# Optimization experiments

Hardware: AMD Instinct MI355X
Metric: run time of the kernel (lower is better)

## Reference

```python
import jax, jax.numpy as jnp
import numpy as np

N_GENES = 15135
K = int(np.ceil(0.5 * N_GENES))  # 7568, PyG TopKPooling ratio=0.5
BS, E, F_IN, H, HF, NC, L = 8, 242160, 64, 128, 512, 2, 3


def setup_inputs() -> dict:
    key = jax.random.key(0)
    ks = jax.random.split(key, 16)
    def lin(k, fin, fout):
        s = 1.0 / np.sqrt(fin)
        return jax.random.normal(k, (fin, fout), jnp.float32) * s
    x = jax.random.normal(ks[0], (BS, N_GENES, F_IN), jnp.float32)
    batch = jnp.zeros((BS,), jnp.int32)
    edge_index = jax.random.randint(ks[1], (2, E), 0, N_GENES, dtype=jnp.int32)
    CAT = L * H
    return {
        "x": x,
        "batch": batch,
        "edge_index": edge_index,
        "W1": lin(ks[2], F_IN, H), "b1": jnp.zeros((H,), jnp.float32),
        "W2": lin(ks[3], H, H),    "b2": jnp.zeros((H,), jnp.float32),
        "W3": lin(ks[4], H, H),    "b3": jnp.zeros((H,), jnp.float32),
        "topk_w": jax.random.normal(ks[5], (CAT,), jnp.float32) / np.sqrt(CAT),
        "fcW": lin(ks[6], CAT, 1), "fcb": jnp.zeros((1,), jnp.float32),
        "lin1W": lin(ks[7], K, HF), "lin1b": jnp.zeros((HF,), jnp.float32),
        "lin2W": lin(ks[8], HF, NC), "lin2b": jnp.zeros((NC,), jnp.float32),
    }


def reference(x, batch, edge_index, W1, b1, W2, b2, W3, b3,
              topk_w, fcW, fcb, lin1W, lin1b, lin2W, lin2b):
    bs = x.shape[0]
    # --- GCN normalization with self-loops (PyG GCNConv defaults) ---
    loop = jnp.arange(N_GENES, dtype=edge_index.dtype)
    src = jnp.concatenate([edge_index[0], loop])
    dst = jnp.concatenate([edge_index[1], loop])
    deg = jnp.zeros((N_GENES,), x.dtype).at[dst].add(1.0)
    dinv = jax.lax.rsqrt(deg)  # deg >= 1 due to self-loops
    norm = dinv[src] * dinv[dst]  # [E+N]

    def gcn(h, W, b):
        h = h @ W                                   # [bs, N, H]
        msg = h[:, src, :] * norm[None, :, None]    # gather + edge weight
        agg = jnp.zeros_like(h).at[:, dst, :].add(msg)  # scatter-add
        return agg + b

    h1 = jax.nn.relu(gcn(x, W1, b1))
    h2 = jax.nn.relu(gcn(h1, W2, b2))
    h3 = jax.nn.relu(gcn(h2, W3, b3))
    # mode='cat': stack on last dim then flatten -> feature order (H, layer)
    xc = jnp.stack([h1, h2, h3], -1).reshape(bs, N_GENES, -1)  # [bs, N, L*H]

    # --- TopKPooling (score = tanh(x.w/||w||), keep top ceil(0.5*N)) ---
    score = jnp.tanh((xc @ topk_w) / jnp.linalg.norm(topk_w))  # [bs, N]
    top_s, perm = jax.lax.top_k(score, K)                       # [bs, K]
    xp = jnp.take_along_axis(xc, perm[..., None], axis=1) * top_s[..., None]

    z = (xp @ fcW + fcb)[..., 0]          # [bs, K]
    h = jax.nn.relu(z @ lin1W + lin1b)    # [bs, HF]; dropout inactive (eval)
    logits = h @ lin2W + lin2b            # [bs, NC]
    return jax.nn.log_softmax(logits, axis=-1)
```

## Files before the change

kernel.cpp:

```cpp
#include <hip/hip_runtime.h>

#define N_G   15135
#define E_N   242160
#define BSZ   8
#define K_TOP 7568
#define NH    128
#define NBIN  65536
#define SUFS  65600

typedef float f4v __attribute__((ext_vector_type(4)));

__global__ void zero_kernel(int* __restrict__ p, int n) {
  int i = blockIdx.x * 1024 + threadIdx.x;
  if (i < n) p[i] = 0;
}

__global__ void count_kernel(const int* __restrict__ ei, int* __restrict__ cnt) {
  int e = blockIdx.x * 256 + threadIdx.x;
  if (e < E_N) atomicAdd(&cnt[ei[E_N + e]], 1);
}

__global__ __launch_bounds__(1024) void scan_kernel(const int* __restrict__ cnt,
                                                    int* __restrict__ rowstart,
                                                    float* __restrict__ dinv,
                                                    int4* __restrict__ rowdesc,
                                                    int* __restrict__ gctr,
                                                    const float* __restrict__ topk_w,
                                                    float* __restrict__ scal) {
  __shared__ int buf[1024];
  __shared__ int base;
  int tid = threadIdx.x;
  int i = blockIdx.x * 1024 + tid;
  int v = (i < N_G) ? cnt[i] : 0;
  float di = 1.0f / sqrtf((float)(v + 1));
  if (i < N_G) dinv[i] = di;
  buf[tid] = v;
  __syncthreads();
  for (int s = 1; s < 1024; s <<= 1) {
    int t = (tid >= s) ? buf[tid - s] : 0;
    __syncthreads();
    buf[tid] += t;
    __syncthreads();
  }
  if (tid == 1023) base = atomicAdd(gctr, buf[1023]);
  __syncthreads();
  if (i < N_G) {
    int rs = base + buf[tid] - v;
    rowstart[i] = rs;
    rowdesc[i] = make_int4(rs, v, __float_as_int(di), 0);
  }
  if (blockIdx.x == 0) {
    __shared__ float fbuf[512];
    if (tid < 512) {
      float w = (tid < 384) ? topk_w[tid] : 0.f;
      fbuf[tid] = w * w;
    }
    __syncthreads();
    for (int s = 256; s > 0; s >>= 1) {
      if (tid < s) fbuf[tid] += fbuf[tid + s];
      __syncthreads();
    }
    if (tid == 0) scal[0] = 1.0f / sqrtf(fbuf[0]);
  }
}

__global__ void fill_kernel(const int* __restrict__ ei, const int* __restrict__ rowstart,
                            const float* __restrict__ dinv, int* __restrict__ fillc,
                            int2* __restrict__ csr) {
  int e = blockIdx.x * 256 + threadIdx.x;
  if (e < E_N) {
    int s = ei[e], d = ei[E_N + e];
    int pos = rowstart[d] + atomicAdd(&fillc[d], 1);
    csr[pos] = make_int2(s, __float_as_int(dinv[s]));
  }
}

template<int CIN, bool BR>
__global__ __launch_bounds__(256, 6) void mm_kernel(const float* __restrict__ A,
                                                    const float* __restrict__ W,
                                                    const float* __restrict__ bias,
                                                    float* __restrict__ out) {
  __shared__ float Bst[32][132];
  __shared__ float Ast2[32][68];
  int tid = threadIdx.x;
  int b = blockIdx.x & 7;
  int ib = blockIdx.x >> 3;
  int rb0 = b * N_G + ib * 64;
  int rmax = N_G - ib * 64;
  int c0 = (tid & 31) * 4;
  int r0 = (tid >> 5) * 8;
  float acc[8][4];
#pragma unroll
  for (int i = 0; i < 8; i++)
#pragma unroll
    for (int j = 0; j < 4; j++) acc[i][j] = 0.f;

  for (int k0 = 0; k0 < CIN; k0 += 32) {
    {
      int koff = (tid & 7) * 4;
      int row = tid >> 3;
#pragma unroll
      for (int p = 0; p < 2; ++p) {
        int r = row + p * 32;
        f4v v = {0.f, 0.f, 0.f, 0.f};
        if (r < rmax) v = __builtin_nontemporal_load((const f4v*)(A + (size_t)(rb0 + r) * CIN + k0 + koff));
        Ast2[koff + 0][r] = v.x; Ast2[koff + 1][r] = v.y;
        Ast2[koff + 2][r] = v.z; Ast2[koff + 3][r] = v.w;
      }
    }
    {
      int cc = (tid & 31) * 4;
      int kr = tid >> 5;
#pragma unroll
      for (int p = 0; p < 4; ++p) {
        int k = kr + p * 8;
        *(float4*)&Bst[k][cc] = *(const float4*)(W + (size_t)(k0 + k) * NH + cc);
      }
    }
    __syncthreads();
#pragma unroll 4
    for (int kk = 0; kk < 32; ++kk) {
      float a[8], bb[4];
      *(float4*)&a[0] = *(const float4*)&Ast2[kk][r0];
      *(float4*)&a[4] = *(const float4*)&Ast2[kk][r0 + 4];
      *(float4*)&bb[0] = *(const float4*)&Bst[kk][c0];
#pragma unroll
      for (int i = 0; i < 8; i++)
#pragma unroll
        for (int j = 0; j < 4; j++)
          acc[i][j] = fmaf(a[i], bb[j], acc[i][j]);
    }
    __syncthreads();
  }
  float b0 = 0.f, b1 = 0.f, b2 = 0.f, b3 = 0.f;
  if (BR) { b0 = bias[c0]; b1 = bias[c0+1]; b2 = bias[c0+2]; b3 = bias[c0+3]; }
#pragma unroll
  for (int i = 0; i < 8; i++) {
    int r = r0 + i;
    if (r < rmax) {
      float4 v;
      if (BR) {
        v.x = fmaxf(acc[i][0] + b0, 0.f); v.y = fmaxf(acc[i][1] + b1, 0.f);
        v.z = fmaxf(acc[i][2] + b2, 0.f); v.w = fmaxf(acc[i][3] + b3, 0.f);
      } else {
        v.x = acc[i][0]; v.y = acc[i][1]; v.z = acc[i][2]; v.w = acc[i][3];
      }
      *(float4*)(out + (size_t)(rb0 + r) * NH + c0) = v;
    }
  }
}

__global__ __launch_bounds__(256) void agg64_f4_kernel(const float* __restrict__ src,
                                                       const int2* __restrict__ csr,
                                                       const int4* __restrict__ rowdesc,
                                                       float* __restrict__ dst) {
  int b = blockIdx.x & 7;
  int chunk = blockIdx.x >> 3;
  int wave = threadIdx.x >> 6, lane = threadIdx.x & 63;
  int d = chunk * 4 + wave;
  if (d >= N_G) return;
  d = __builtin_amdgcn_readfirstlane(d);
  int slot = lane >> 4, li = lane & 15;
  int4 rd = rowdesc[d];
  int n = rd.y;
  float dv = __int_as_float(rd.z);
  const float* sb = src + (size_t)b * N_G * 64;
  const int2* ce = csr + rd.x;
  auto sel4 = [&](int a0, int a1, int a2, int a3) {
    int s01 = (slot & 1) ? a1 : a0;
    int s23 = (slot & 1) ? a3 : a2;
    return (slot & 2) ? s23 : s01;
  };
  f4v acc0 = {0.f, 0.f, 0.f, 0.f}, acc1 = {0.f, 0.f, 0.f, 0.f};
  {
    f4v sv = *(const f4v*)(sb + (size_t)d * 64 + li * 4);
    float ws = (slot == 0) ? dv : 0.f;
    acc0.x = fmaf(ws, sv.x, acc0.x); acc0.y = fmaf(ws, sv.y, acc0.y);
    acc0.z = fmaf(ws, sv.z, acc0.z); acc0.w = fmaf(ws, sv.w, acc0.w);
  }
  int l = 0;
  for (; l + 8 <= n; l += 8) {
    int2 p[8];
#pragma unroll
    for (int k = 0; k < 8; ++k) p[k] = ce[l + k];
    int s0 = sel4(p[0].x, p[1].x, p[2].x, p[3].x);
    int s1 = sel4(p[4].x, p[5].x, p[6].x, p[7].x);
    float w0 = __int_as_float(sel4(p[0].y, p[1].y, p[2].y, p[3].y));
    float w1 = __int_as_float(sel4(p[4].y, p[5].y, p[6].y, p[7].y));
    f4v v0 = *(const f4v*)(sb + (size_t)s0 * 64 + li * 4);
    f4v v1 = *(const f4v*)(sb + (size_t)s1 * 64 + li * 4);
    acc0.x = fmaf(w0, v0.x, acc0.x); acc0.y = fmaf(w0, v0.y, acc0.y);
    acc0.z = fmaf(w0, v0.z, acc0.z); acc0.w = fmaf(w0, v0.w, acc0.w);
    acc1.x = fmaf(w1, v1.x, acc1.x); acc1.y = fmaf(w1, v1.y, acc1.y);
    acc1.z = fmaf(w1, v1.z, acc1.z); acc1.w = fmaf(w1, v1.w, acc1.w);
  }
  for (; l < n; ++l) {
    int2 p = ce[l];
    float w = (slot == 0) ? __int_as_float(p.y) : 0.f;
    f4v v = *(const f4v*)(sb + (size_t)p.x * 64 + li * 4);
    acc0.x = fmaf(w, v.x, acc0.x); acc0.y = fmaf(w, v.y, acc0.y);
    acc0.z = fmaf(w, v.z, acc0.z); acc0.w = fmaf(w, v.w, acc0.w);
  }
  f4v a;
  a.x = acc0.x + acc1.x; a.y = acc0.y + acc1.y;
  a.z = acc0.z + acc1.z; a.w = acc0.w + acc1.w;
  a.x += __shfl_xor(a.x, 16); a.y += __shfl_xor(a.y, 16);
  a.z += __shfl_xor(a.z, 16); a.w += __shfl_xor(a.w, 16);
  a.x += __shfl_xor(a.x, 32); a.y += __shfl_xor(a.y, 32);
  a.z += __shfl_xor(a.z, 32); a.w += __shfl_xor(a.w, 32);
  if (slot == 0) {
    f4v r;
    r.x = dv * a.x; r.y = dv * a.y; r.z = dv * a.z; r.w = dv * a.w;
    __builtin_nontemporal_store(r, (f4v*)(dst + ((size_t)b * N_G + d) * 64 + li * 4));
  }
}

template<int MODE>
__global__ __launch_bounds__(256) void agg128_f4_kernel(const float* __restrict__ hw,
                                                        const int2* __restrict__ csr,
                                                        const int4* __restrict__ rowdesc,
                                                        const float* __restrict__ bias,
                                                        const float* __restrict__ h1,
                                                        const float* __restrict__ h2,
                                                        const float* __restrict__ topk_w,
                                                        const float* __restrict__ fcW,
                                                        const float* __restrict__ scal,
                                                        float* __restrict__ hout,
                                                        float* __restrict__ score,
                                                        float* __restrict__ d2a,
                                                        unsigned* __restrict__ keys,
                                                        int* __restrict__ hist) {
  int b = blockIdx.x & 7;
  int chunk = blockIdx.x >> 3;
  int wave = threadIdx.x >> 6, lane = threadIdx.x & 63;
  int d0 = chunk * 8 + wave * 2;
  if (d0 >= N_G) return;
  d0 = __builtin_amdgcn_readfirstlane(d0);
  int d1i = d0 + 1;
  int has1 = (d1i < N_G);
  int dB = has1 ? d1i : d0;
  int half = lane >> 5, li = lane & 31;
  int4 rdA = rowdesc[d0];
  int4 rdB = rowdesc[dB];
  int nA = rdA.y, nB = has1 ? rdB.y : 0;
  float dvA = __int_as_float(rdA.z);
  float dvB = __int_as_float(rdB.z);
  const float* sb = hw + (size_t)b * N_G * NH;
  const int2* ceA = csr + rdA.x;
  const int2* ceB = csr + rdB.x;
  auto sel2 = [&](int a0, int a1) { return half ? a1 : a0; };
  f4v aA0 = {0.f,0.f,0.f,0.f}, aA1 = {0.f,0.f,0.f,0.f};
  f4v aB0 = {0.f,0.f,0.f,0.f}, aB1 = {0.f,0.f,0.f,0.f};
  {
    f4v sv = *(const f4v*)(sb + (size_t)d0 * NH + li * 4);
    float ws = (half == 0) ? dvA : 0.f;
    aA0.x = fmaf(ws, sv.x, aA0.x); aA0.y = fmaf(ws, sv.y, aA0.y);
    aA0.z = fmaf(ws, sv.z, aA0.z); aA0.w = fmaf(ws, sv.w, aA0.w);
    f4v svb = *(const f4v*)(sb + (size_t)dB * NH + li * 4);
    float wsb = (half == 0 && has1) ? dvB : 0.f;
    aB0.x = fmaf(wsb, svb.x, aB0.x); aB0.y = fmaf(wsb, svb.y, aB0.y);
    aB0.z = fmaf(wsb, svb.z, aB0.z); aB0.w = fmaf(wsb, svb.w, aB0.w);
  }
  auto batch8 = [&](const int2* ce, int l, f4v& c0, f4v& c1) {
    int2 p[8];
#pragma unroll
    for (int k = 0; k < 8; ++k) p[k] = ce[l + k];
    int s0 = sel2(p[0].x, p[1].x), s1 = sel2(p[2].x, p[3].x);
    int s2 = sel2(p[4].x, p[5].x), s3 = sel2(p[6].x, p[7].x);
    float w0 = __int_as_float(sel2(p[0].y, p[1].y));
    float w1 = __int_as_float(sel2(p[2].y, p[3].y));
    float w2 = __int_as_float(sel2(p[4].y, p[5].y));
    float w3 = __int_as_float(sel2(p[6].y, p[7].y));
    f4v v0 = *(const f4v*)(sb + (size_t)s0 * NH + li * 4);
    f4v v1 = *(const f4v*)(sb + (size_t)s1 * NH + li * 4);
    f4v v2 = *(const f4v*)(sb + (size_t)s2 * NH + li * 4);
    f4v v3 = *(const f4v*)(sb + (size_t)s3 * NH + li * 4);
    c0.x = fmaf(w0, v0.x, c0.x); c0.y = fmaf(w0, v0.y, c0.y);
    c0.z = fmaf(w0, v0.z, c0.z); c0.w = fmaf(w0, v0.w, c0.w);
    c1.x = fmaf(w1, v1.x, c1.x); c1.y = fmaf(w1, v1.y, c1.y);
    c1.z = fmaf(w1, v1.z, c1.z); c1.w = fmaf(w1, v1.w, c1.w);
    c0.x = fmaf(w2, v2.x, c0.x); c0.y = fmaf(w2, v2.y, c0.y);
    c0.z = fmaf(w2, v2.z, c0.z); c0.w = fmaf(w2, v2.w, c0.w);
    c1.x = fmaf(w3, v3.x, c1.x); c1.y = fmaf(w3, v3.y, c1.y);
    c1.z = fmaf(w3, v3.z, c1.z); c1.w = fmaf(w3, v3.w, c1.w);
  };
  int lA = 0, lB = 0;
  while (lA + 8 <= nA && lB + 8 <= nB) {
    int2 pA[8], pB[8];
#pragma unroll
    for (int k = 0; k < 8; ++k) pA[k] = ceA[lA + k];
#pragma unroll
    for (int k = 0; k < 8; ++k) pB[k] = ceB[lB + k];
    int sa0 = sel2(pA[0].x, pA[1].x), sa1 = sel2(pA[2].x, pA[3].x);
    int sa2 = sel2(pA[4].x, pA[5].x), sa3 = sel2(pA[6].x, pA[7].x);
    int sb0_ = sel2(pB[0].x, pB[1].x), sb1_ = sel2(pB[2].x, pB[3].x);
    int sb2_ = sel2(pB[4].x, pB[5].x), sb3_ = sel2(pB[6].x, pB[7].x);
    float wa0 = __int_as_float(sel2(pA[0].y, pA[1].y));
    float wa1 = __int_as_float(sel2(pA[2].y, pA[3].y));
    float wa2 = __int_as_float(sel2(pA[4].y, pA[5].y));
    float wa3 = __int_as_float(sel2(pA[6].y, pA[7].y));
    float wb0 = __int_as_float(sel2(pB[0].y, pB[1].y));
    float wb1 = __int_as_float(sel2(pB[2].y, pB[3].y));
    float wb2 = __int_as_float(sel2(pB[4].y, pB[5].y));
    float wb3 = __int_as_float(sel2(pB[6].y, pB[7].y));
    f4v va0 = *(const f4v*)(sb + (size_t)sa0 * NH + li * 4);
    f4v va1 = *(const f4v*)(sb + (size_t)sa1 * NH + li * 4);
    f4v va2 = *(const f4v*)(sb + (size_t)sa2 * NH + li * 4);
    f4v va3 = *(const f4v*)(sb + (size_t)sa3 * NH + li * 4);
    f4v vb0 = *(const f4v*)(sb + (size_t)sb0_ * NH + li * 4);
    f4v vb1 = *(const f4v*)(sb + (size_t)sb1_ * NH + li * 4);
    f4v vb2 = *(const f4v*)(sb + (size_t)sb2_ * NH + li * 4);
    f4v vb3 = *(const f4v*)(sb + (size_t)sb3_ * NH + li * 4);
    aA0.x = fmaf(wa0, va0.x, aA0.x); aA0.y = fmaf(wa0, va0.y, aA0.y);
    aA0.z = fmaf(wa0, va0.z, aA0.z); aA0.w = fmaf(wa0, va0.w, aA0.w);
    aA1.x = fmaf(wa1, va1.x, aA1.x); aA1.y = fmaf(wa1, va1.y, aA1.y);
    aA1.z = fmaf(wa1, va1.z, aA1.z); aA1.w = fmaf(wa1, va1.w, aA1.w);
    aA0.x = fmaf(wa2, va2.x, aA0.x); aA0.y = fmaf(wa2, va2.y, aA0.y);
    aA0.z = fmaf(wa2, va2.z, aA0.z); aA0.w = fmaf(wa2, va2.w, aA0.w);
    aA1.x = fmaf(wa3, va3.x, aA1.x); aA1.y = fmaf(wa3, va3.y, aA1.y);
    aA1.z = fmaf(wa3, va3.z, aA1.z); aA1.w = fmaf(wa3, va3.w, aA1.w);
    aB0.x = fmaf(wb0, vb0.x, aB0.x); aB0.y = fmaf(wb0, vb0.y, aB0.y);
    aB0.z = fmaf(wb0, vb0.z, aB0.z); aB0.w = fmaf(wb0, vb0.w, aB0.w);
    aB1.x = fmaf(wb1, vb1.x, aB1.x); aB1.y = fmaf(wb1, vb1.y, aB1.y);
    aB1.z = fmaf(wb1, vb1.z, aB1.z); aB1.w = fmaf(wb1, vb1.w, aB1.w);
    aB0.x = fmaf(wb2, vb2.x, aB0.x); aB0.y = fmaf(wb2, vb2.y, aB0.y);
    aB0.z = fmaf(wb2, vb2.z, aB0.z); aB0.w = fmaf(wb2, vb2.w, aB0.w);
    aB1.x = fmaf(wb3, vb3.x, aB1.x); aB1.y = fmaf(wb3, vb3.y, aB1.y);
    aB1.z = fmaf(wb3, vb3.z, aB1.z); aB1.w = fmaf(wb3, vb3.w, aB1.w);
    lA += 8; lB += 8;
  }
  for (; lA + 8 <= nA; lA += 8) batch8(ceA, lA, aA0, aA1);
  for (; lB + 8 <= nB; lB += 8) batch8(ceB, lB, aB0, aB1);
  while (lA < nA || lB < nB) {
    int hasA = (lA < nA), hasB = (lB < nB);
    int sA = hasA ? ceA[lA].x : d0;
    int wAi = hasA ? ceA[lA].y : 0;
    int sB = hasB ? ceB[lB].x : d0;
    int wBi = hasB ? ceB[lB].y : 0;
    int s = half ? sB : sA;
    float wa = (half == 0 && hasA) ? __int_as_float(wAi) : 0.f;
    float wb = (half == 1 && hasB) ? __int_as_float(wBi) : 0.f;
    f4v v = *(const f4v*)(sb + (size_t)s * NH + li * 4);
    aA0.x = fmaf(wa, v.x, aA0.x); aA0.y = fmaf(wa, v.y, aA0.y);
    aA0.z = fmaf(wa, v.z, aA0.z); aA0.w = fmaf(wa, v.w, aA0.w);
    aB0.x = fmaf(wb, v.x, aB0.x); aB0.y = fmaf(wb, v.y, aB0.y);
    aB0.z = fmaf(wb, v.z, aB0.z); aB0.w = fmaf(wb, v.w, aB0.w);
    lA += hasA; lB += hasB;
  }
  f4v aA, aB;
  aA.x = aA0.x + aA1.x; aA.y = aA0.y + aA1.y;
  aA.z = aA0.z + aA1.z; aA.w = aA0.w + aA1.w;
  aB.x = aB0.x + aB1.x; aB.y = aB0.y + aB1.y;
  aB.z = aB0.z + aB1.z; aB.w = aB0.w + aB1.w;
  aA.x += __shfl_xor(aA.x, 32); aA.y += __shfl_xor(aA.y, 32);
  aA.z += __shfl_xor(aA.z, 32); aA.w += __shfl_xor(aA.w, 32);
  aB.x += __shfl_xor(aB.x, 32); aB.y += __shfl_xor(aB.y, 32);
  aB.z += __shfl_xor(aB.z, 32); aB.w += __shfl_xor(aB.w, 32);

  f4v bb = *(const f4v*)(bias + li * 4);
  float dv = half ? dvB : dvA;
  f4v av;
  av.x = half ? aB.x : aA.x; av.y = half ? aB.y : aA.y;
  av.z = half ? aB.z : aA.z; av.w = half ? aB.w : aA.w;
  f4v r;
  r.x = fmaxf(fmaf(dv, av.x, bb.x), 0.f);
  r.y = fmaxf(fmaf(dv, av.y, bb.y), 0.f);
  r.z = fmaxf(fmaf(dv, av.z, bb.z), 0.f);
  r.w = fmaxf(fmaf(dv, av.w, bb.w), 0.f);
  int dsel = half ? dB : d0;

  if constexpr (MODE == 0) {
    if (half == 0 || has1)
      __builtin_nontemporal_store(r, (f4v*)(hout + ((size_t)b * N_G + dsel) * NH + li * 4));
  } else {
    size_t rb = ((size_t)b * N_G + dsel) * NH + li * 4;
    f4v u1 = __builtin_nontemporal_load((const f4v*)(h1 + rb));
    f4v u2 = __builtin_nontemporal_load((const f4v*)(h2 + rb));
    const float* twp = topk_w + li * 12;
    const float* fwp = fcW + li * 12;
    f4v ta = *(const f4v*)(twp + 0), tb2 = *(const f4v*)(twp + 4), tc = *(const f4v*)(twp + 8);
    f4v fa = *(const f4v*)(fwp + 0), fb = *(const f4v*)(fwp + 4), fc = *(const f4v*)(fwp + 8);
    float d1 = u1.x * ta.x + u2.x * ta.y + r.x * ta.z
             + u1.y * ta.w + u2.y * tb2.x + r.y * tb2.y
             + u1.z * tb2.z + u2.z * tb2.w + r.z * tc.x
             + u1.w * tc.y + u2.w * tc.z + r.w * tc.w;
    float d2 = u1.x * fa.x + u2.x * fa.y + r.x * fa.z
             + u1.y * fa.w + u2.y * fb.x + r.y * fb.y
             + u1.z * fb.z + u2.z * fb.w + r.z * fc.x
             + u1.w * fc.y + u2.w * fc.z + r.w * fc.w;
#pragma unroll
    for (int sh = 16; sh > 0; sh >>= 1) {
      d1 += __shfl_down(d1, sh, 32);
      d2 += __shfl_down(d2, sh, 32);
    }
    if (li == 0 && (half == 0 || has1)) {
      int gw = b * N_G + dsel;
      float scv = tanhf(d1 * scal[0]);
      score[gw] = scv;
      d2a[gw] = d2;
      unsigned u = __float_as_uint(scv);
      unsigned k32 = (u & 0x80000000u) ? ~u : (u | 0x80000000u);
      keys[gw] = k32;
      atomicAdd(&hist[b * NBIN + (int)(k32 >> 16)], 1);
    }
  }
}

__global__ __launch_bounds__(1024) void suffix_kernel(const int* __restrict__ hist,
                                                      int* __restrict__ suf) {
  __shared__ int buf[1024];
  int b = blockIdx.x;
  const int* hb = hist + b * NBIN;
  int* sb = suf + b * SUFS;
  int t = threadIdx.x;
  int base = t * 64;
  int s = 0;
  for (int k = 0; k < 64; ++k) s += hb[base + k];
  buf[t] = s;
  __syncthreads();
  for (int off = 1; off < 1024; off <<= 1) {
    int v = (t + off < 1024) ? buf[t + off] : 0;
    __syncthreads();
    buf[t] += v;
    __syncthreads();
  }
  int acc = buf[t] - s;
  if (t == 0) sb[NBIN] = 0;
  for (int k = 63; k >= 0; --k) {
    acc += hb[base + k];
    sb[base + k] = acc;
  }
}

__global__ void scatter_kernel(const unsigned* __restrict__ keys, int* __restrict__ hist,
                               const int* __restrict__ suf, int2* __restrict__ bucket) {
  int b = blockIdx.y;
  int i = blockIdx.x * 256 + threadIdx.x;
  if (i >= N_G) return;
  unsigned k = keys[b * N_G + i];
  int bin = (int)(k >> 16);
  int old = atomicSub(&hist[b * NBIN + bin], 1);
  int pos = suf[b * SUFS + bin + 1] + old - 1;
  bucket[b * N_G + pos] = make_int2((int)k, i);
}

__global__ void rank_z_kernel(const unsigned* __restrict__ keys, const int* __restrict__ suf,
                              const int2* __restrict__ bucket, const float* __restrict__ score,
                              const float* __restrict__ d2a, const float* __restrict__ fcb,
                              float* __restrict__ z) {
  int b = blockIdx.y;
  int i = blockIdx.x * 256 + threadIdx.x;
  if (i >= N_G) return;
  int gw = b * N_G + i;
  unsigned k = keys[gw];
  int bin = (int)(k >> 16);
  int lo = suf[b * SUFS + bin + 1];
  int hi = suf[b * SUFS + bin];
  int r = lo;
  const int2* bk = bucket + b * N_G;
  for (int p = lo; p < hi; ++p) {
    int2 e = bk[p];
    unsigned kj = (unsigned)e.x;
    r += (kj > k || (kj == k && e.y < i)) ? 1 : 0;
  }
  if (r < K_TOP) z[b * K_TOP + r] = fmaf(score[gw], d2a[gw], fcb[0]);
}

__global__ __launch_bounds__(256) void lin1_kernel(const float* __restrict__ z,
                                                   const float* __restrict__ W,
                                                   float* __restrict__ hpre) {
  __shared__ float zb[237];
  int b = blockIdx.y, rs = blockIdx.x;
  int r0 = rs * 237;
  int rn = K_TOP - r0; if (rn > 237) rn = 237;
  for (int q = threadIdx.x; q < rn; q += 256) zb[q] = z[b * K_TOP + r0 + q];
  __syncthreads();
  int c = threadIdx.x;
  float a0 = 0.f, a1 = 0.f;
  for (int r = 0; r < rn; ++r) {
    float zz = zb[r];
    const float* wr = W + (size_t)(r0 + r) * 512;
    a0 = fmaf(zz, wr[c], a0);
    a1 = fmaf(zz, wr[c + 256], a1);
  }
  atomicAdd(&hpre[b * 512 + c], a0);
  atomicAdd(&hpre[b * 512 + c + 256], a1);
}

__global__ __launch_bounds__(128) void lin2_kernel(const float* __restrict__ hpre,
                                                   const float* __restrict__ l1b,
                                                   const float* __restrict__ W2,
                                                   const float* __restrict__ l2b,
                                                   float* __restrict__ out) {
  int b = blockIdx.x, tid = threadIdx.x;
  float a0 = 0.f, a1 = 0.f;
  for (int j = tid; j < 512; j += 128) {
    float t = fmaxf(hpre[b * 512 + j] + l1b[j], 0.f);
    a0 = fmaf(t, W2[j * 2 + 0], a0);
    a1 = fmaf(t, W2[j * 2 + 1], a1);
  }
#pragma unroll
  for (int s = 32; s > 0; s >>= 1) {
    a0 += __shfl_down(a0, s);
    a1 += __shfl_down(a1, s);
  }
  __shared__ float red[2][2];
  if ((tid & 63) == 0) { red[tid >> 6][0] = a0; red[tid >> 6][1] = a1; }
  __syncthreads();
  if (tid == 0) {
    float l0 = red[0][0] + red[1][0] + l2b[0];
    float l1 = red[0][1] + red[1][1] + l2b[1];
    float m = fmaxf(l0, l1);
    float lse = m + logf(expf(l0 - m) + expf(l1 - m));
    out[b * 2 + 0] = l0 - lse;
    out[b * 2 + 1] = l1 - lse;
  }
}

extern "C" void kernel_launch(void* const* d_in, const int* in_sizes, int n_in,
                              void* d_out, int out_size, void* d_ws, size_t ws_size,
                              hipStream_t stream) {
  const float* x   = (const float*)d_in[0];
  const int*   ei  = (const int*)d_in[2];
  const float* W1  = (const float*)d_in[3];
  const float* b1  = (const float*)d_in[4];
  const float* W2  = (const float*)d_in[5];
  const float* b2  = (const float*)d_in[6];
  const float* W3  = (const float*)d_in[7];
  const float* b3  = (const float*)d_in[8];
  const float* tkw = (const float*)d_in[9];
  const float* fcW = (const float*)d_in[10];
  const float* fcb = (const float*)d_in[11];
  const float* l1W = (const float*)d_in[12];
  const float* l1b = (const float*)d_in[13];
  const float* l2W = (const float*)d_in[14];
  const float* l2b = (const float*)d_in[15];
  float* out = (float*)d_out;

  char* ws = (char*)d_ws;
  size_t off = 0;
  auto alloc = [&](size_t bytes) {
    char* p = ws + off;
    off += (bytes + 255) & ~(size_t)255;
    return p;
  };
  int*   cnt   = (int*)alloc(15136 * 4);
  int*   fillc = (int*)alloc(15136 * 4);
  int*   gctr  = (int*)alloc(256);
  float* hpre  = (float*)alloc(4096 * 4);
  int*   hist  = (int*)alloc((size_t)BSZ * NBIN * 4);
  int*   rowstart = (int*)alloc(15136 * 4);
  float* dinv  = (float*)alloc(15136 * 4);
  int4*  rowdesc = (int4*)alloc(15136 * 16);
  float* scal  = (float*)alloc(64);
  float* z     = (float*)alloc((size_t)BSZ * K_TOP * 4);
  float* score = (float*)alloc(121088 * 4);
  float* d2a   = (float*)alloc(121088 * 4);
  unsigned* keys = (unsigned*)alloc(121088 * 4);
  int*   suf   = (int*)alloc((size_t)BSZ * SUFS * 4);
  int2*  bucket = (int2*)alloc(121088 * 8);
  int2*  csr   = (int2*)alloc((size_t)E_N * 8);
  float* ax = (float*)alloc((size_t)BSZ * N_G * 64 * 4);
  float* hw = (float*)alloc((size_t)BSZ * N_G * NH * 4);
  float* h1 = (float*)alloc((size_t)BSZ * N_G * NH * 4);
  float* h2 = (float*)alloc((size_t)BSZ * N_G * NH * 4);
  (void)ws_size; (void)in_sizes; (void)n_in; (void)out_size;

  int zero_n = (int)(((char*)rowstart - (char*)cnt) / 4);
  zero_kernel<<<(zero_n + 1023) / 1024, 1024, 0, stream>>>(cnt, zero_n);
  count_kernel<<<(E_N + 255) / 256, 256, 0, stream>>>(ei, cnt);
  scan_kernel<<<(N_G + 1023) / 1024, 1024, 0, stream>>>(cnt, rowstart, dinv, rowdesc, gctr, tkw, scal);
  fill_kernel<<<(E_N + 255) / 256, 256, 0, stream>>>(ei, rowstart, dinv, fillc, csr);

  dim3 mmg(8 * 237);
  int aggblocks  = 8 * ((N_G + 3) / 4);
  int aggblocks2 = 8 * ((N_G + 7) / 8);

  agg64_f4_kernel<<<aggblocks, 256, 0, stream>>>(x, csr, rowdesc, ax);
  mm_kernel<64, true><<<mmg, 256, 0, stream>>>(ax, W1, b1, h1);
  mm_kernel<128, false><<<mmg, 256, 0, stream>>>(h1, W2, nullptr, hw);
  agg128_f4_kernel<0><<<aggblocks2, 256, 0, stream>>>(hw, csr, rowdesc, b2,
                                                      nullptr, nullptr, nullptr, nullptr, nullptr,
                                                      h2, nullptr, nullptr, nullptr, nullptr);
  mm_kernel<128, false><<<mmg, 256, 0, stream>>>(h2, W3, nullptr, hw);
  agg128_f4_kernel<1><<<aggblocks2, 256, 0, stream>>>(hw, csr, rowdesc, b3,
                                                      h1, h2, tkw, fcW, scal,
                                                      nullptr, score, d2a, keys, hist);

  dim3 ng((N_G + 255) / 256, BSZ);
  suffix_kernel<<<BSZ, 1024, 0, stream>>>(hist, suf);
  scatter_kernel<<<ng, 256, 0, stream>>>(keys, hist, suf, bucket);
  rank_z_kernel<<<ng, 256, 0, stream>>>(keys, suf, bucket, score, d2a, fcb, z);

  dim3 l1g(32, BSZ);
  lin1_kernel<<<l1g, 256, 0, stream>>>(z, l1W, hpre);
  lin2_kernel<<<BSZ, 128, 0, stream>>>(hpre, l1b, l2W, l2b, out);
}
```

Measured before the change: 616.8 us.

## Store layer-3 transform in fp16 and batch lin1 across graphs

The third GCN layer's matmul output is written as fp16, and a new aggregation+score kernel gathers fp16 rows, so gather traffic for that layer is halved. It processes one node per wave with 16-lane slots and four edges in flight. lin1 now handles all 8 batch rows per block, so each weight row is read once instead of eight times. The agg128 kernel is simplified to its non-score mode. The fp16 intermediate reduces precision and could perturb top-k ordering near ties.

```diff
diff --git a/kernel.cpp b/kernel.cpp
--- a/kernel.cpp
+++ b/kernel.cpp
@@ -1,4 +1,5 @@
 #include <hip/hip_runtime.h>
+#include <hip/hip_fp16.h>
 
 #define N_G   15135
 #define E_N   242160
@@ -9,6 +10,7 @@
 #define SUFS  65600
 
 typedef float f4v __attribute__((ext_vector_type(4)));
+typedef unsigned int u4v __attribute__((ext_vector_type(4)));
 
 __global__ void zero_kernel(int* __restrict__ p, int n) {
   int i = blockIdx.x * 1024 + threadIdx.x;
@@ -75,11 +77,11 @@
   }
 }
 
-template<int CIN, bool BR>
+template<int CIN, bool BR, bool H16>
 __global__ __launch_bounds__(256, 6) void mm_kernel(const float* __restrict__ A,
                                                     const float* __restrict__ W,
                                                     const float* __restrict__ bias,
-                                                    float* __restrict__ out) {
+                                                    void* __restrict__ outv) {
   __shared__ float Bst[32][132];
   __shared__ float Ast2[32][68];
   int tid = threadIdx.x;
@@ -138,14 +140,21 @@
   for (int i = 0; i < 8; i++) {
     int r = r0 + i;
     if (r < rmax) {
-      float4 v;
-      if (BR) {
-        v.x = fmaxf(acc[i][0] + b0, 0.f); v.y = fmaxf(acc[i][1] + b1, 0.f);
-        v.z = fmaxf(acc[i][2] + b2, 0.f); v.w = fmaxf(acc[i][3] + b3, 0.f);
+      if (H16) {
+        __half2 pr[2];
+        pr[0] = __floats2half2_rn(acc[i][0], acc[i][1]);
+        pr[1] = __floats2half2_rn(acc[i][2], acc[i][3]);
+        *(uint2*)((__half*)outv + (size_t)(rb0 + r) * NH + c0) = *(uint2*)pr;
       } else {
-        v.x = acc[i][0]; v.y = acc[i][1]; v.z = acc[i][2]; v.w = acc[i][3];
+        float4 v;
+        if (BR) {
+          v.x = fmaxf(acc[i][0] + b0, 0.f); v.y = fmaxf(acc[i][1] + b1, 0.f);
+          v.z = fmaxf(acc[i][2] + b2, 0.f); v.w = fmaxf(acc[i][3] + b3, 0.f);
+        } else {
+          v.x = acc[i][0]; v.y = acc[i][1]; v.z = acc[i][2]; v.w = acc[i][3];
+        }
+        *(float4*)((float*)outv + (size_t)(rb0 + r) * NH + c0) = v;
       }
-      *(float4*)(out + (size_t)(rb0 + r) * NH + c0) = v;
     }
   }
 }
@@ -215,21 +224,11 @@
   }
 }
 
-template<int MODE>
 __global__ __launch_bounds__(256) void agg128_f4_kernel(const float* __restrict__ hw,
                                                         const int2* __restrict__ csr,
                                                         const int4* __restrict__ rowdesc,
                                                         const float* __restrict__ bias,
-                                                        const float* __restrict__ h1,
-                                                        const float* __restrict__ h2,
-                                                        const float* __restrict__ topk_w,
-                                                        const float* __restrict__ fcW,
-                                                        const float* __restrict__ scal,
-                                                        float* __restrict__ hout,
-                                                        float* __restrict__ score,
-                                                        float* __restrict__ d2a,
-                                                        unsigned* __restrict__ keys,
-                                                        int* __restrict__ hist) {
+                                                        float* __restrict__ hout) {
   int b = blockIdx.x & 7;
   int chunk = blockIdx.x >> 3;
   int wave = threadIdx.x >> 6, lane = threadIdx.x & 63;
@@ -286,47 +285,8 @@
   };
   int lA = 0, lB = 0;
   while (lA + 8 <= nA && lB + 8 <= nB) {
-    int2 pA[8], pB[8];
-#pragma unroll
-    for (int k = 0; k < 8; ++k) pA[k] = ceA[lA + k];
-#pragma unroll
-    for (int k = 0; k < 8; ++k) pB[k] = ceB[lB + k];
-    int sa0 = sel2(pA[0].x, pA[1].x), sa1 = sel2(pA[2].x, pA[3].x);
-    int sa2 = sel2(pA[4].x, pA[5].x), sa3 = sel2(pA[6].x, pA[7].x);
-    int sb0_ = sel2(pB[0].x, pB[1].x), sb1_ = sel2(pB[2].x, pB[3].x);
-    int sb2_ = sel2(pB[4].x, pB[5].x), sb3_ = sel2(pB[6].x, pB[7].x);
-    float wa0 = __int_as_float(sel2(pA[0].y, pA[1].y));
-    float wa1 = __int_as_float(sel2(pA[2].y, pA[3].y));
-    float wa2 = __int_as_float(sel2(pA[4].y, pA[5].y));
-    float wa3 = __int_as_float(sel2(pA[6].y, pA[7].y));
-    float wb0 = __int_as_float(sel2(pB[0].y, pB[1].y));
-    float wb1 = __int_as_float(sel2(pB[2].y, pB[3].y));
-    float wb2 = __int_as_float(sel2(pB[4].y, pB[5].y));
-    float wb3 = __int_as_float(sel2(pB[6].y, pB[7].y));
-    f4v va0 = *(const f4v*)(sb + (size_t)sa0 * NH + li * 4);
-    f4v va1 = *(const f4v*)(sb + (size_t)sa1 * NH + li * 4);
-    f4v va2 = *(const f4v*)(sb + (size_t)sa2 * NH + li * 4);
-    f4v va3 = *(const f4v*)(sb + (size_t)sa3 * NH + li * 4);
-    f4v vb0 = *(const f4v*)(sb + (size_t)sb0_ * NH + li * 4);
-    f4v vb1 = *(const f4v*)(sb + (size_t)sb1_ * NH + li * 4);
-    f4v vb2 = *(const f4v*)(sb + (size_t)sb2_ * NH + li * 4);
-    f4v vb3 = *(const f4v*)(sb + (size_t)sb3_ * NH + li * 4);
-    aA0.x = fmaf(wa0, va0.x, aA0.x); aA0.y = fmaf(wa0, va0.y, aA0.y);
-    aA0.z = fmaf(wa0, va0.z, aA0.z); aA0.w = fmaf(wa0, va0.w, aA0.w);
-    aA1.x = fmaf(wa1, va1.x, aA1.x); aA1.y = fmaf(wa1, va1.y, aA1.y);
-    aA1.z = fmaf(wa1, va1.z, aA1.z); aA1.w = fmaf(wa1, va1.w, aA1.w);
-    aA0.x = fmaf(wa2, va2.x, aA0.x); aA0.y = fmaf(wa2, va2.y, aA0.y);
-    aA0.z = fmaf(wa2, va2.z, aA0.z); aA0.w = fmaf(wa2, va2.w, aA0.w);
-    aA1.x = fmaf(wa3, va3.x, aA1.x); aA1.y = fmaf(wa3, va3.y, aA1.y);
-    aA1.z = fmaf(wa3, va3.z, aA1.z); aA1.w = fmaf(wa3, va3.w, aA1.w);
-    aB0.x = fmaf(wb0, vb0.x, aB0.x); aB0.y = fmaf(wb0, vb0.y, aB0.y);
-    aB0.z = fmaf(wb0, vb0.z, aB0.z); aB0.w = fmaf(wb0, vb0.w, aB0.w);
-    aB1.x = fmaf(wb1, vb1.x, aB1.x); aB1.y = fmaf(wb1, vb1.y, aB1.y);
-    aB1.z = fmaf(wb1, vb1.z, aB1.z); aB1.w = fmaf(wb1, vb1.w, aB1.w);
-    aB0.x = fmaf(wb2, vb2.x, aB0.x); aB0.y = fmaf(wb2, vb2.y, aB0.y);
-    aB0.z = fmaf(wb2, vb2.z, aB0.z); aB0.w = fmaf(wb2, vb2.w, aB0.w);
-    aB1.x = fmaf(wb3, vb3.x, aB1.x); aB1.y = fmaf(wb3, vb3.y, aB1.y);
-    aB1.z = fmaf(wb3, vb3.z, aB1.z); aB1.w = fmaf(wb3, vb3.w, aB1.w);
+    batch8(ceA, lA, aA0, aA1);
+    batch8(ceB, lB, aB0, aB1);
     lA += 8; lB += 8;
   }
   for (; lA + 8 <= nA; lA += 8) batch8(ceA, lA, aA0, aA1);
@@ -368,41 +328,120 @@
   r.z = fmaxf(fmaf(dv, av.z, bb.z), 0.f);
   r.w = fmaxf(fmaf(dv, av.w, bb.w), 0.f);
   int dsel = half ? dB : d0;
-
-  if constexpr (MODE == 0) {
-    if (half == 0 || has1)
-      __builtin_nontemporal_store(r, (f4v*)(hout + ((size_t)b * N_G + dsel) * NH + li * 4));
-  } else {
-    size_t rb = ((size_t)b * N_G + dsel) * NH + li * 4;
-    f4v u1 = __builtin_nontemporal_load((const f4v*)(h1 + rb));
-    f4v u2 = __builtin_nontemporal_load((const f4v*)(h2 + rb));
-    const float* twp = topk_w + li * 12;
-    const float* fwp = fcW + li * 12;
-    f4v ta = *(const f4v*)(twp + 0), tb2 = *(const f4v*)(twp + 4), tc = *(const f4v*)(twp + 8);
-    f4v fa = *(const f4v*)(fwp + 0), fb = *(const f4v*)(fwp + 4), fc = *(const f4v*)(fwp + 8);
-    float d1 = u1.x * ta.x + u2.x * ta.y + r.x * ta.z
-             + u1.y * ta.w + u2.y * tb2.x + r.y * tb2.y
-             + u1.z * tb2.z + u2.z * tb2.w + r.z * tc.x
-             + u1.w * tc.y + u2.w * tc.z + r.w * tc.w;
-    float d2 = u1.x * fa.x + u2.x * fa.y + r.x * fa.z
-             + u1.y * fa.w + u2.y * fb.x + r.y * fb.y
-             + u1.z * fb.z + u2.z * fb.w + r.z * fc.x
-             + u1.w * fc.y + u2.w * fc.z + r.w * fc.w;
-#pragma unroll
-    for (int sh = 16; sh > 0; sh >>= 1) {
-      d1 += __shfl_down(d1, sh, 32);
-      d2 += __shfl_down(d2, sh, 32);
-    }
-    if (li == 0 && (half == 0 || has1)) {
-      int gw = b * N_G + dsel;
-      float scv = tanhf(d1 * scal[0]);
-      score[gw] = scv;
-      d2a[gw] = d2;
-      unsigned u = __float_as_uint(scv);
-      unsigned k32 = (u & 0x80000000u) ? ~u : (u | 0x80000000u);
-      keys[gw] = k32;
-      atomicAdd(&hist[b * NBIN + (int)(k32 >> 16)], 1);
-    }
+  if (half == 0 || has1)
+    __builtin_nontemporal_store(r, (f4v*)(hout + ((size_t)b * N_G + dsel) * NH + li * 4));
+}
+
+__global__ __launch_bounds__(256) void agg128h_score_kernel(
+    const __half* __restrict__ hwh,
+    const int2* __restrict__ csr,
+    const int4* __restrict__ rowdesc,
+    const float* __restrict__ bias,
+    const float* __restrict__ h1,
+    const float* __restrict__ h2,
+    const float* __restrict__ topk_w,
+    const float* __restrict__ fcW,
+    const float* __restrict__ scal,
+    float* __restrict__ score,
+    float* __restrict__ d2a,
+    unsigned* __restrict__ keys,
+    int* __restrict__ hist) {
+  int b = blockIdx.x & 7;
+  int chunk = blockIdx.x >> 3;
+  int wave = threadIdx.x >> 6, lane = threadIdx.x & 63;
+  int d = chunk * 4 + wave;
+  if (d >= N_G) return;
+  d = __builtin_amdgcn_readfirstlane(d);
+  int slot = lane >> 4, li = lane & 15;
+  int4 rd = rowdesc[d];
+  int n = rd.y;
+  float dv = __int_as_float(rd.z);
+  const __half* sb = hwh + (size_t)b * N_G * NH;
+  const int2* ce = csr + rd.x;
+  auto sel4 = [&](int a0, int a1, int a2, int a3) {
+    int s01 = (slot & 1) ? a1 : a0;
+    int s23 = (slot & 1) ? a3 : a2;
+    return (slot & 2) ? s23 : s01;
+  };
+  float a0[8], a1[8];
+#pragma unroll
+  for (int j = 0; j < 8; ++j) { a0[j] = 0.f; a1[j] = 0.f; }
+  auto gacc = [&](int s, float w, float* acc) {
+    u4v raw = *(const u4v*)(sb + (size_t)s * NH + li * 8);
+    unsigned q0 = raw.x, q1 = raw.y, q2 = raw.z, q3 = raw.w;
+    float2 f0 = __half22float2(*(const __half2*)&q0);
+    float2 f1 = __half22float2(*(const __half2*)&q1);
+    float2 f2 = __half22float2(*(const __half2*)&q2);
+    float2 f3 = __half22float2(*(const __half2*)&q3);
+    acc[0] = fmaf(w, f0.x, acc[0]); acc[1] = fmaf(w, f0.y, acc[1]);
+    acc[2] = fmaf(w, f1.x, acc[2]); acc[3] = fmaf(w, f1.y, acc[3]);
+    acc[4] = fmaf(w, f2.x, acc[4]); acc[5] = fmaf(w, f2.y, acc[5]);
+    acc[6] = fmaf(w, f3.x, acc[6]); acc[7] = fmaf(w, f3.y, acc[7]);
+  };
+  gacc(d, (slot == 0) ? dv : 0.f, a0);
+  int l = 0;
+  for (; l + 8 <= n; l += 8) {
+    int2 p[8];
+#pragma unroll
+    for (int k = 0; k < 8; ++k) p[k] = ce[l + k];
+    int s0 = sel4(p[0].x, p[1].x, p[2].x, p[3].x);
+    int s1 = sel4(p[4].x, p[5].x, p[6].x, p[7].x);
+    float w0 = __int_as_float(sel4(p[0].y, p[1].y, p[2].y, p[3].y));
+    float w1 = __int_as_float(sel4(p[4].y, p[5].y, p[6].y, p[7].y));
+    gacc(s0, w0, a0);
+    gacc(s1, w1, a1);
+  }
+  for (; l < n; ++l) {
+    int2 p = ce[l];
+    gacc(p.x, (slot == 0) ? __int_as_float(p.y) : 0.f, a0);
+  }
+  float a[8];
+#pragma unroll
+  for (int j = 0; j < 8; ++j) {
+    a[j] = a0[j] + a1[j];
+    a[j] += __shfl_xor(a[j], 16);
+    a[j] += __shfl_xor(a[j], 32);
+  }
+  size_t rb = ((size_t)b * N_G + d) * NH + li * 8;
+  f4v u1a = __builtin_nontemporal_load((const f4v*)(h1 + rb));
+  f4v u1b = __builtin_nontemporal_load((const f4v*)(h1 + rb + 4));
+  f4v u2a = __builtin_nontemporal_load((const f4v*)(h2 + rb));
+  f4v u2b = __builtin_nontemporal_load((const f4v*)(h2 + rb + 4));
+  f4v bba = *(const f4v*)(bias + li * 8);
+  f4v bbb = *(const f4v*)(bias + li * 8 + 4);
+  float r[8];
+  r[0] = fmaxf(fmaf(dv, a[0], bba.x), 0.f);
+  r[1] = fmaxf(fmaf(dv, a[1], bba.y), 0.f);
+  r[2] = fmaxf(fmaf(dv, a[2], bba.z), 0.f);
+  r[3] = fmaxf(fmaf(dv, a[3], bba.w), 0.f);
+  r[4] = fmaxf(fmaf(dv, a[4], bbb.x), 0.f);
+  r[5] = fmaxf(fmaf(dv, a[5], bbb.y), 0.f);
+  r[6] = fmaxf(fmaf(dv, a[6], bbb.z), 0.f);
+  r[7] = fmaxf(fmaf(dv, a[7], bbb.w), 0.f);
+  float u1[8] = {u1a.x, u1a.y, u1a.z, u1a.w, u1b.x, u1b.y, u1b.z, u1b.w};
+  float u2[8] = {u2a.x, u2a.y, u2a.z, u2a.w, u2b.x, u2b.y, u2b.z, u2b.w};
+  const float* tw = topk_w + li * 24;
+  const float* fw = fcW + li * 24;
+  float d1 = 0.f, d2 = 0.f;
+#pragma unroll
+  for (int j = 0; j < 8; ++j) {
+    d1 += u1[j] * tw[j * 3] + u2[j] * tw[j * 3 + 1] + r[j] * tw[j * 3 + 2];
+    d2 += u1[j] * fw[j * 3] + u2[j] * fw[j * 3 + 1] + r[j] * fw[j * 3 + 2];
+  }
+#pragma unroll
+  for (int sh = 8; sh > 0; sh >>= 1) {
+    d1 += __shfl_down(d1, sh, 16);
+    d2 += __shfl_down(d2, sh, 16);
+  }
+  if (lane == 0) {
+    int gw = b * N_G + d;
+    float scv = tanhf(d1 * scal[0]);
+    score[gw] = scv;
+    d2a[gw] = d2;
+    unsigned u = __float_as_uint(scv);
+    unsigned k32 = (u & 0x80000000u) ? ~u : (u | 0x80000000u);
+    keys[gw] = k32;
+    atomicAdd(&hist[b * NBIN + (int)(k32 >> 16)], 1);
   }
 }
 
@@ -469,22 +508,34 @@
 __global__ __launch_bounds__(256) void lin1_kernel(const float* __restrict__ z,
                                                    const float* __restrict__ W,
                                                    float* __restrict__ hpre) {
-  __shared__ float zb[237];
-  int b = blockIdx.y, rs = blockIdx.x;
+  __shared__ float zb[8][237];
+  int rs = blockIdx.x;
   int r0 = rs * 237;
   int rn = K_TOP - r0; if (rn > 237) rn = 237;
-  for (int q = threadIdx.x; q < rn; q += 256) zb[q] = z[b * K_TOP + r0 + q];
+  for (int t = threadIdx.x; t < 8 * rn; t += 256) {
+    int bb = t / rn, rr = t - bb * rn;
+    zb[bb][rr] = z[bb * K_TOP + r0 + rr];
+  }
   __syncthreads();
   int c = threadIdx.x;
-  float a0 = 0.f, a1 = 0.f;
+  float a[8][2];
+#pragma unroll
+  for (int bb = 0; bb < 8; ++bb) { a[bb][0] = 0.f; a[bb][1] = 0.f; }
   for (int r = 0; r < rn; ++r) {
-    float zz = zb[r];
     const float* wr = W + (size_t)(r0 + r) * 512;
-    a0 = fmaf(zz, wr[c], a0);
-    a1 = fmaf(zz, wr[c + 256], a1);
-  }
-  atomicAdd(&hpre[b * 512 + c], a0);
-  atomicAdd(&hpre[b * 512 + c + 256], a1);
+    float w0 = wr[c], w1 = wr[c + 256];
+#pragma unroll
+    for (int bb = 0; bb < 8; ++bb) {
+      float zz = zb[bb][r];
+      a[bb][0] = fmaf(zz, w0, a[bb][0]);
+      a[bb][1] = fmaf(zz, w1, a[bb][1]);
+    }
+  }
+#pragma unroll
+  for (int bb = 0; bb < 8; ++bb) {
+    atomicAdd(&hpre[bb * 512 + c], a[bb][0]);
+    atomicAdd(&hpre[bb * 512 + c + 256], a[bb][1]);
+  }
 }
 
 __global__ __launch_bounds__(128) void lin2_kernel(const float* __restrict__ hpre,
@@ -577,22 +628,19 @@
   int aggblocks2 = 8 * ((N_G + 7) / 8);
 
   agg64_f4_kernel<<<aggblocks, 256, 0, stream>>>(x, csr, rowdesc, ax);
-  mm_kernel<64, true><<<mmg, 256, 0, stream>>>(ax, W1, b1, h1);
-  mm_kernel<128, false><<<mmg, 256, 0, stream>>>(h1, W2, nullptr, hw);
-  agg128_f4_kernel<0><<<aggblocks2, 256, 0, stream>>>(hw, csr, rowdesc, b2,
-                                                      nullptr, nullptr, nullptr, nullptr, nullptr,
-                                                      h2, nullptr, nullptr, nullptr, nullptr);
-  mm_kernel<128, false><<<mmg, 256, 0, stream>>>(h2, W3, nullptr, hw);
-  agg128_f4_kernel<1><<<aggblocks2, 256, 0, stream>>>(hw, csr, rowdesc, b3,
+  mm_kernel<64, true, false><<<mmg, 256, 0, stream>>>(ax, W1, b1, h1);
+  mm_kernel<128, false, false><<<mmg, 256, 0, stream>>>(h1, W2, nullptr, hw);
+  agg128_f4_kernel<<<aggblocks2, 256, 0, stream>>>(hw, csr, rowdesc, b2, h2);
+  mm_kernel<128, false, true><<<mmg, 256, 0, stream>>>(h2, W3, nullptr, hw);
+  agg128h_score_kernel<<<aggblocks, 256, 0, stream>>>((const __half*)hw, csr, rowdesc, b3,
                                                       h1, h2, tkw, fcW, scal,
-                                                      nullptr, score, d2a, keys, hist);
+                                                      score, d2a, keys, hist);
 
   dim3 ng((N_G + 255) / 256, BSZ);
   suffix_kernel<<<BSZ, 1024, 0, stream>>>(hist, suf);
   scatter_kernel<<<ng, 256, 0, stream>>>(keys, hist, suf, bucket);
   rank_z_kernel<<<ng, 256, 0, stream>>>(keys, suf, bucket, score, d2a, fcb, z);
 
-  dim3 l1g(32, BSZ);
-  lin1_kernel<<<l1g, 256, 0, stream>>>(z, l1W, hpre);
+  lin1_kernel<<<32, 256, 0, stream>>>(z, l1W, hpre);
   lin2_kernel<<<BSZ, 128, 0, stream>>>(hpre, l1b, l2W, l2b, out);
 }
```

Result: slower. 650.8 us (+5.5%).
